# Performance work log

Hardware: AMD Instinct MI355X
Metric: run time of the kernel (lower is better)

Reference implementation:

```python
import jax, jax.numpy as jnp
import numpy as np
from jax import lax

NOISE_STD = 0.0005
ALPHA = 0.1
B, S, I, H, O = 128, 2000, 8, 512, 2
NUM_EXC, NUM_INH = 384, 128


def setup_inputs() -> dict:
    key = jax.random.key(0)
    ks = jax.random.split(key, 6)
    return {
        "input": jax.random.normal(ks[0], (B, S, I), dtype=jnp.float32),
        "noise": jax.random.normal(ks[1], (B, S, H), dtype=jnp.float32),
        "wi": jax.random.normal(ks[2], (I, H), dtype=jnp.float32) / np.sqrt(I),
        # excitatory rows in [0, 0.5], inhibitory rows in [-0.5, 0] (Dale's law)
        "wrec_exc": jax.random.uniform(ks[3], (NUM_EXC, H), dtype=jnp.float32, minval=0.0, maxval=0.5),
        "wrec_inh": jax.random.uniform(ks[4], (NUM_INH, H), dtype=jnp.float32, minval=-0.5, maxval=0.0),
        "wout": jax.random.normal(ks[5], (H, O), dtype=jnp.float32) / np.sqrt(H),
        "h0": jnp.zeros((H,), dtype=jnp.float32),
    }


def reference(input, noise, wi, wrec_exc, wrec_inh, wout, h0):
    batch = input.shape[0]
    # wrec rows: [exc sources; inh sources]
    wrec = jnp.concatenate([wrec_exc, wrec_inh], axis=0)  # [H, H]
    r0 = jnp.tanh(h0)  # [H]
    out0 = jnp.broadcast_to(r0 @ wout, (batch, wout.shape[1]))  # output[:, 0]
    h_init = jnp.broadcast_to(h0, (batch, h0.shape[0]))  # [B, H]
    # precompute input projection for steps 0..S-2 (last step's input unused)
    xproj = jnp.einsum("bsi,ih->sbh", input[:, :-1], wi)  # [S-1, B, H]
    noise_t = jnp.transpose(noise[:, :-1], (1, 0, 2))  # [S-1, B, H]

    def step(h, inp):
        x_t, n_t = inp
        r = jnp.tanh(h)
        h_new = h + NOISE_STD * n_t + ALPHA * (-h + r @ wrec.T + x_t)
        return h_new, jnp.tanh(h_new) @ wout  # emit output[:, i+1]

    _, outs = lax.scan(step, h_init, (xproj, noise_t))  # outs: [S-1, B, O]
    output = jnp.concatenate([out0[None], outs], axis=0)  # [S, B, O]
    return jnp.transpose(output, (1, 0, 2))  # [B, S, O]
```

## Files before the change

### kernel.cpp

```cpp
#include <hip/hip_runtime.h>
#include <cmath>


constexpr int kS = 2000, kI = 8, kH = 512, kO = 2;
constexpr float kNoiseStd = 0.0005f, kAlpha = 0.1f;

constexpr int GROUPS = 8;
constexpr int NSPL   = 2;
constexpr int JS     = 256;
constexpr int NTHR   = 512;
constexpr int NBLK   = GROUPS * NSPL;
constexpr int RSLOT  = 8192;

typedef _Float16 half8  __attribute__((ext_vector_type(8)));
typedef float    floatx4 __attribute__((ext_vector_type(4)));
typedef unsigned uintx4  __attribute__((ext_vector_type(4)));

#define MFMA16(A, B, C) __builtin_amdgcn_mfma_f32_16x16x32_f16((A), (B), (C), 0, 0, 0)
#define PIN8(a) asm volatile("" : "+v"((a)[0]), "+v"((a)[1]), "+v"((a)[2]), "+v"((a)[3]), \
                                   "+v"((a)[4]), "+v"((a)[5]), "+v"((a)[6]), "+v"((a)[7]))

static __device__ __forceinline__ unsigned ld_flag(const unsigned* p) {
  return __hip_atomic_load(p, __ATOMIC_RELAXED, __HIP_MEMORY_SCOPE_AGENT);
}
static __device__ __forceinline__ void st_flag(unsigned* p, unsigned v) {
  __hip_atomic_store(p, v, __ATOMIC_RELAXED, __HIP_MEMORY_SCOPE_AGENT);
}

static __device__ __forceinline__ float fast_tanh(float x) {
  const float ax = __builtin_fabsf(x);
  const float e = __builtin_amdgcn_exp2f(2.8853900817779268f * ax);
  const float r = __builtin_amdgcn_rcpf(e + 1.0f);
  return __builtin_copysignf(__builtin_fmaf(-2.0f, r, 1.0f), x);
}

__global__ __launch_bounds__(NTHR, 1) void rnn_k(
    const float* __restrict__ inp,
    const float* __restrict__ noise,
    const float* __restrict__ wi,
    const float* __restrict__ wexc,
    const float* __restrict__ winh,
    const float* __restrict__ wout,
    const float* __restrict__ h0,
    float* __restrict__ out,
    _Float16* __restrict__ rbuf,
    unsigned* __restrict__ flags)
{
  const int bid = blockIdx.x;
  const int g = bid & 7;
  const int c = bid >> 3;
  const int tid = threadIdx.x;
  const int w = tid >> 6;
  const int lane = tid & 63;
  const int l15 = lane & 15;
  const int lhi = lane >> 4;

  const int j0 = c * JS + w * 32 + l15;
  const int j1 = j0 + 16;
  const int ktp = c * 8 + w;
  const int jsub0 = l15 >> 3, jsub1 = 2 + (l15 >> 3), vv = l15 & 7;

  unsigned myXcd;
  asm volatile("s_getreg_b32 %0, hwreg(HW_REG_XCC_ID)" : "=s"(myXcd));
  myXcd &= 0x7fffu;

  __shared__ _Float16 ldsA[2][RSLOT];
  __shared__ half8 ws_wout[16][64];
  __shared__ float ldsIN[16][kI];

  half8 wfo0[8], wfo1[8], wfp0[8], wfp1[8];
  {
    const float* wr0 = (j0 < 384) ? (wexc + (size_t)j0 * kH) : (winh + (size_t)(j0 - 384) * kH);
    const float* wr1 = (j1 < 384) ? (wexc + (size_t)j1 * kH) : (winh + (size_t)(j1 - 384) * kH);
    const int ko = (c * 8) * 32 + lhi * 8;
    const int kp = ((c ^ 1) * 8) * 32 + lhi * 8;
#pragma unroll
    for (int t = 0; t < 8; ++t) {
      half8 a, b, d, e;
#pragma unroll
      for (int v = 0; v < 8; ++v) {
        a[v] = (_Float16)wr0[ko + t * 32 + v];
        b[v] = (_Float16)wr1[ko + t * 32 + v];
        d[v] = (_Float16)wr0[kp + t * 32 + v];
        e[v] = (_Float16)wr1[kp + t * 32 + v];
      }
      wfo0[t] = a; wfo1[t] = b; wfp0[t] = d; wfp1[t] = e;
    }
    PIN8(wfo0); PIN8(wfo1); PIN8(wfp0); PIN8(wfp1);
  }

  float wiv0[8], wiv1[8];
#pragma unroll
  for (int i = 0; i < 8; ++i) { wiv0[i] = wi[i * kH + j0]; wiv1[i] = wi[i * kH + j1]; }

  if (c == 0 && w < 4) {
#pragma unroll
    for (int t = 0; t < 4; ++t) {
      const int kt = w * 4 + t;
      const int k0 = kt * 32 + lhi * 8;
      half8 hv;
#pragma unroll
      for (int v = 0; v < 8; ++v)
        hv[v] = (l15 < kO) ? (_Float16)wout[(size_t)(k0 + v) * kO + l15] : (_Float16)0.f;
      ws_wout[kt][lane] = hv;
    }
  }

  float hq0[4], hq1[4];
  {
    const float h00 = h0[j0], h01 = h0[j1];
#pragma unroll
    for (int q = 0; q < 4; ++q) { hq0[q] = h00; hq1[q] = h01; }
    const _Float16 r00 = (_Float16)fast_tanh(h00);
    const _Float16 r01 = (_Float16)fast_tanh(h01);
#pragma unroll
    for (int q = 0; q < 4; ++q) {
      const int bb = lhi * 4 + q;
      ldsA[0][ktp * 512 + (bb + 16 * jsub0) * 8 + vv] = r00;
      ldsA[0][ktp * 512 + (bb + 16 * jsub1) * 8 + vv] = r01;
    }
    const uintx4 pub = *(const uintx4*)((const char*)&ldsA[0][0] + ktp * 1024 + lane * 16);
    char* dst = (char*)rbuf + (size_t)(0 * GROUPS + g) * (RSLOT * 2) + ktp * 1024 + lane * 16;
    asm volatile("global_store_dwordx4 %0, %1, off sc0 sc1" :: "v"(dst), "v"(pub) : "memory");
  }
  __syncthreads();
  if (tid == 0) st_flag(&flags[(0 * GROUPS + g) * NSPL + c], (myXcd << 16) | 1u);

  bool sameXcd;
  {
    unsigned pf;
    const unsigned* fp = &flags[(0 * GROUPS + g) * NSPL + (c ^ 1)];
    do { pf = ld_flag(fp); } while ((pf & 0xffffu) < 1u);
    sameXcd = ((pf >> 16) == myXcd);
    asm volatile("" ::: "memory");
  }

  for (int s = 0; s < kS; ++s) {
    const int cur = s & 1;
    const bool lastS = (s == kS - 1);
    if (lastS && c != 0) break;

    if (c == 0 && w == 7 && s > 0) {
      floatx4 oa = {0,0,0,0}, ob = {0,0,0,0};
      const char* bprev = (const char*)&ldsA[cur ^ 1][0];
#pragma unroll
      for (int kt = 0; kt < 16; kt += 2) {
        const half8 f0 = *(const half8*)(bprev + kt * 1024 + lane * 16);
        const half8 f1 = *(const half8*)(bprev + (kt + 1) * 1024 + lane * 16);
        oa = MFMA16(f0, ws_wout[kt][lane], oa);
        ob = MFMA16(f1, ws_wout[kt + 1][lane], ob);
      }
      if (l15 < kO) {
#pragma unroll
        for (int q = 0; q < 4; ++q)
          out[((size_t)(g * 16 + lhi * 4 + q) * kS + (s - 1)) * kO + l15] = oa[q] + ob[q];
      }
    }

    float nz0[4], nz1[4];
    float inv = 0.f;
    if (!lastS) {
#pragma unroll
      for (int q = 0; q < 4; ++q) {
        const int b = g * 16 + lhi * 4 + q;
        nz0[q] = noise[((size_t)b * kS + s) * kH + j0];
        nz1[q] = noise[((size_t)b * kS + s) * kH + j1];
      }
      if (w == 2 || w == 3) {
        const int ii = tid - 128;
        inv = inp[((size_t)(g * 16 + (ii >> 3)) * kS + s) * kI + (ii & 7)];
      }
    }

    {
      const unsigned need = (unsigned)(s + 1);
      const unsigned* fp = &flags[(cur * GROUPS + g) * NSPL + (c ^ 1)];
      while ((ld_flag(fp) & 0xffffu) < need) {}
      asm volatile("" ::: "memory");
    }

    uintx4 pv;
    {
      const char* src = (const char*)rbuf + (size_t)(cur * GROUPS + g) * (RSLOT * 2)
                        + (c ^ 1) * 8192 + tid * 16;
      if (sameXcd)
        asm volatile("global_load_dwordx4 %0, %1, off sc0" : "=&v"(pv) : "v"(src) : "memory");
      else
        asm volatile("global_load_dwordx4 %0, %1, off sc0 sc1" : "=&v"(pv) : "v"(src) : "memory");
    }

    floatx4 a00 = {0,0,0,0}, a01 = {0,0,0,0}, a10 = {0,0,0,0}, a11 = {0,0,0,0};
    const char* base = (const char*)&ldsA[cur][0];
    const char* baseO = base + c * 8192;
    const char* baseP = base + (c ^ 1) * 8192;
#pragma unroll
    for (int t = 0; t < 8; t += 2) {
      const half8 f0 = *(const half8*)(baseO + t * 1024 + lane * 16);
      const half8 f1 = *(const half8*)(baseO + (t + 1) * 1024 + lane * 16);
      a00 = MFMA16(f0, wfo0[t], a00);
      a10 = MFMA16(f0, wfo1[t], a10);
      a01 = MFMA16(f1, wfo0[t + 1], a01);
      a11 = MFMA16(f1, wfo1[t + 1], a11);
    }
    __builtin_amdgcn_sched_barrier(0);
    asm volatile("s_waitcnt vmcnt(0)" : "+v"(pv) :: "memory");
    *(uintx4*)((char*)&ldsA[cur][0] + (c ^ 1) * 8192 + tid * 16) = pv;
    if (!lastS && (w == 2 || w == 3)) {
      const int ii = tid - 128;
      ldsIN[ii >> 3][ii & 7] = inv;
    }
    __syncthreads();

#pragma unroll
    for (int t = 0; t < 8; t += 2) {
      const half8 f0 = *(const half8*)(baseP + t * 1024 + lane * 16);
      const half8 f1 = *(const half8*)(baseP + (t + 1) * 1024 + lane * 16);
      a00 = MFMA16(f0, wfp0[t], a00);
      a10 = MFMA16(f0, wfp1[t], a10);
      a01 = MFMA16(f1, wfp0[t + 1], a01);
      a11 = MFMA16(f1, wfp1[t + 1], a11);
    }

    if (!lastS) {
      _Float16* lA = &ldsA[cur ^ 1][0];
#pragma unroll
      for (int q = 0; q < 4; ++q) {
        const int bb = lhi * 4 + q;
        const floatx4 iv0 = *(const floatx4*)&ldsIN[bb][0];
        const floatx4 iv1 = *(const floatx4*)&ldsIN[bb][4];
        float x0 = 0.f, x1 = 0.f;
#pragma unroll
        for (int i = 0; i < 4; ++i) {
          x0 = fmaf(iv0[i], wiv0[i], x0); x0 = fmaf(iv1[i], wiv0[i + 4], x0);
          x1 = fmaf(iv0[i], wiv1[i], x1); x1 = fmaf(iv1[i], wiv1[i + 4], x1);
        }
        const float y0 = a00[q] + a01[q], y1 = a10[q] + a11[q];
        const float h0n = hq0[q] + kNoiseStd * nz0[q] + kAlpha * (-hq0[q] + y0 + x0);
        const float h1n = hq1[q] + kNoiseStd * nz1[q] + kAlpha * (-hq1[q] + y1 + x1);
        hq0[q] = h0n; hq1[q] = h1n;
        lA[ktp * 512 + (bb + 16 * jsub0) * 8 + vv] = (_Float16)fast_tanh(h0n);
        lA[ktp * 512 + (bb + 16 * jsub1) * 8 + vv] = (_Float16)fast_tanh(h1n);
      }
      const uintx4 pub = *(const uintx4*)((const char*)lA + ktp * 1024 + lane * 16);
      char* dst = (char*)rbuf + (size_t)((cur ^ 1) * GROUPS + g) * (RSLOT * 2)
                  + ktp * 1024 + lane * 16;
      if (sameXcd)
        asm volatile("global_store_dwordx4 %0, %1, off sc0" :: "v"(dst), "v"(pub) : "memory");
      else
        asm volatile("global_store_dwordx4 %0, %1, off sc0 sc1" :: "v"(dst), "v"(pub) : "memory");
    }
    __syncthreads();
    if (!lastS && tid == 0)
      st_flag(&flags[((cur ^ 1) * GROUPS + g) * NSPL + c], (unsigned)(s + 2));
  }

  if (c == 0 && w == 7) {
    const char* bfin = (const char*)&ldsA[(kS - 1) & 1][0];
    floatx4 oa = {0,0,0,0}, ob = {0,0,0,0};
#pragma unroll
    for (int kt = 0; kt < 16; kt += 2) {
      const half8 f0 = *(const half8*)(bfin + kt * 1024 + lane * 16);
      const half8 f1 = *(const half8*)(bfin + (kt + 1) * 1024 + lane * 16);
      oa = MFMA16(f0, ws_wout[kt][lane], oa);
      ob = MFMA16(f1, ws_wout[kt + 1][lane], ob);
    }
    if (l15 < kO) {
#pragma unroll
      for (int q = 0; q < 4; ++q)
        out[((size_t)(g * 16 + lhi * 4 + q) * kS + (kS - 1)) * kO + l15] = oa[q] + ob[q];
    }
  }
}

extern "C" void kernel_launch(void* const* d_in, const int* in_sizes, int n_in,
                              void* d_out, int out_size, void* d_ws, size_t ws_size,
                              hipStream_t stream) {
  const float* inp   = (const float*)d_in[0];
  const float* noise = (const float*)d_in[1];
  const float* wi    = (const float*)d_in[2];
  const float* wexc  = (const float*)d_in[3];
  const float* winh  = (const float*)d_in[4];
  const float* wout  = (const float*)d_in[5];
  const float* h0    = (const float*)d_in[6];

  _Float16* rbuf = (_Float16*)d_ws;
  const size_t rbytes = (size_t)2 * GROUPS * RSLOT * sizeof(_Float16);
  unsigned* flags = (unsigned*)((char*)d_ws + rbytes);

  hipMemsetAsync(flags, 0, 2 * GROUPS * NSPL * sizeof(unsigned), stream);
  rnn_k<<<NBLK, NTHR, 0, stream>>>(inp, noise, wi, wexc, winh, wout, h0,
                                   (float*)d_out, rbuf, flags);
}
```

Measured before the change: 4.531 ms.

## Remove mid-step barrier by loading peer fragments directly into registers

Each wave now loads the peer half of the recurrent activations straight from global memory into MFMA operand registers, instead of staging them in LDS and waiting on a mid-step __syncthreads. The LDS activation buffer becomes triple-buffered and the input slice is prefetched one step ahead into a double-buffered LDS array, so the per-step barrier is no longer needed. The goal is to shorten the serial critical path of each recurrence step. The cost is eight extra 16-byte global loads per lane per step and more live registers.

```diff
diff --git a/kernel.cpp b/kernel.cpp
--- a/kernel.cpp
+++ b/kernel.cpp
@@ -64,9 +64,9 @@
   asm volatile("s_getreg_b32 %0, hwreg(HW_REG_XCC_ID)" : "=s"(myXcd));
   myXcd &= 0x7fffu;
 
-  __shared__ _Float16 ldsA[2][RSLOT];
+  __shared__ _Float16 ldsA[3][RSLOT];
   __shared__ half8 ws_wout[16][64];
-  __shared__ float ldsIN[16][kI];
+  __shared__ float ldsIN[2][16][kI];
 
   half8 wfo0[8], wfo1[8], wfp0[8], wfp1[8];
   {
@@ -104,6 +104,11 @@
         hv[v] = (l15 < kO) ? (_Float16)wout[(size_t)(k0 + v) * kO + l15] : (_Float16)0.f;
       ws_wout[kt][lane] = hv;
     }
+  }
+
+  if (w == 2 || w == 3) {
+    const int ii = tid - 128;
+    ldsIN[0][ii >> 3][ii & 7] = inp[((size_t)(g * 16 + (ii >> 3)) * kS + 0) * kI + (ii & 7)];
   }
 
   float hq0[4], hq1[4];
@@ -135,6 +140,9 @@
     asm volatile("" ::: "memory");
   }
 
+  const char* base = (const char*)&ldsA[0][0];
+  int s3p = 2, s3c = 0, s3n = 1;
+
   for (int s = 0; s < kS; ++s) {
     const int cur = s & 1;
     const bool lastS = (s == kS - 1);
@@ -142,7 +150,7 @@
 
     if (c == 0 && w == 7 && s > 0) {
       floatx4 oa = {0,0,0,0}, ob = {0,0,0,0};
-      const char* bprev = (const char*)&ldsA[cur ^ 1][0];
+      const char* bprev = base + s3p * 16384;
 #pragma unroll
       for (int kt = 0; kt < 16; kt += 2) {
         const half8 f0 = *(const half8*)(bprev + kt * 1024 + lane * 16);
@@ -158,7 +166,7 @@
     }
 
     float nz0[4], nz1[4];
-    float inv = 0.f;
+    float invN = 0.f;
     if (!lastS) {
 #pragma unroll
       for (int q = 0; q < 4; ++q) {
@@ -166,10 +174,10 @@
         nz0[q] = noise[((size_t)b * kS + s) * kH + j0];
         nz1[q] = noise[((size_t)b * kS + s) * kH + j1];
       }
-      if (w == 2 || w == 3) {
-        const int ii = tid - 128;
-        inv = inp[((size_t)(g * 16 + (ii >> 3)) * kS + s) * kI + (ii & 7)];
-      }
+    }
+    if (s < kS - 2 && (w == 2 || w == 3)) {
+      const int ii = tid - 128;
+      invN = inp[((size_t)(g * 16 + (ii >> 3)) * kS + (s + 1)) * kI + (ii & 7)];
     }
 
     {
@@ -180,19 +188,51 @@
     }
 
     uintx4 pv;
+    half8 rf0, rf1, rf2, rf3, rf4, rf5, rf6, rf7;
     {
-      const char* src = (const char*)rbuf + (size_t)(cur * GROUPS + g) * (RSLOT * 2)
-                        + (c ^ 1) * 8192 + tid * 16;
-      if (sameXcd)
-        asm volatile("global_load_dwordx4 %0, %1, off sc0" : "=&v"(pv) : "v"(src) : "memory");
-      else
-        asm volatile("global_load_dwordx4 %0, %1, off sc0 sc1" : "=&v"(pv) : "v"(src) : "memory");
+      const char* phalf = (const char*)rbuf + (size_t)(cur * GROUPS + g) * (RSLOT * 2)
+                          + (c ^ 1) * 8192;
+      const char* srcpv = phalf + tid * 16;
+      const char* srcrf = phalf + lane * 16;
+      const char* srcrh = srcrf + 4096;
+      if (sameXcd) {
+        asm volatile("global_load_dwordx4 %0, %1, off sc0" : "=&v"(pv) : "v"(srcpv) : "memory");
+        asm volatile(
+          "global_load_dwordx4 %0, %4, off sc0\n\t"
+          "global_load_dwordx4 %1, %4, off offset:1024 sc0\n\t"
+          "global_load_dwordx4 %2, %4, off offset:2048 sc0\n\t"
+          "global_load_dwordx4 %3, %4, off offset:3072 sc0"
+          : "=&v"(rf0), "=&v"(rf1), "=&v"(rf2), "=&v"(rf3)
+          : "v"(srcrf) : "memory");
+        asm volatile(
+          "global_load_dwordx4 %0, %4, off sc0\n\t"
+          "global_load_dwordx4 %1, %4, off offset:1024 sc0\n\t"
+          "global_load_dwordx4 %2, %4, off offset:2048 sc0\n\t"
+          "global_load_dwordx4 %3, %4, off offset:3072 sc0"
+          : "=&v"(rf4), "=&v"(rf5), "=&v"(rf6), "=&v"(rf7)
+          : "v"(srcrh) : "memory");
+      } else {
+        asm volatile("global_load_dwordx4 %0, %1, off sc0 sc1" : "=&v"(pv) : "v"(srcpv) : "memory");
+        asm volatile(
+          "global_load_dwordx4 %0, %4, off sc0 sc1\n\t"
+          "global_load_dwordx4 %1, %4, off offset:1024 sc0 sc1\n\t"
+          "global_load_dwordx4 %2, %4, off offset:2048 sc0 sc1\n\t"
+          "global_load_dwordx4 %3, %4, off offset:3072 sc0 sc1"
+          : "=&v"(rf0), "=&v"(rf1), "=&v"(rf2), "=&v"(rf3)
+          : "v"(srcrf) : "memory");
+        asm volatile(
+          "global_load_dwordx4 %0, %4, off sc0 sc1\n\t"
+          "global_load_dwordx4 %1, %4, off offset:1024 sc0 sc1\n\t"
+          "global_load_dwordx4 %2, %4, off offset:2048 sc0 sc1\n\t"
+          "global_load_dwordx4 %3, %4, off offset:3072 sc0 sc1"
+          : "=&v"(rf4), "=&v"(rf5), "=&v"(rf6), "=&v"(rf7)
+          : "v"(srcrh) : "memory");
+      }
     }
 
     floatx4 a00 = {0,0,0,0}, a01 = {0,0,0,0}, a10 = {0,0,0,0}, a11 = {0,0,0,0};
-    const char* base = (const char*)&ldsA[cur][0];
-    const char* baseO = base + c * 8192;
-    const char* baseP = base + (c ^ 1) * 8192;
+    const char* bA = base + s3c * 16384;
+    const char* baseO = bA + c * 8192;
 #pragma unroll
     for (int t = 0; t < 8; t += 2) {
       const half8 f0 = *(const half8*)(baseO + t * 1024 + lane * 16);
@@ -203,31 +243,40 @@
       a11 = MFMA16(f1, wfo1[t + 1], a11);
     }
     __builtin_amdgcn_sched_barrier(0);
-    asm volatile("s_waitcnt vmcnt(0)" : "+v"(pv) :: "memory");
-    *(uintx4*)((char*)&ldsA[cur][0] + (c ^ 1) * 8192 + tid * 16) = pv;
-    if (!lastS && (w == 2 || w == 3)) {
+    asm volatile("s_waitcnt vmcnt(0)"
+                 : "+v"(pv), "+v"(rf0), "+v"(rf1), "+v"(rf2), "+v"(rf3),
+                   "+v"(rf4), "+v"(rf5), "+v"(rf6), "+v"(rf7) :: "memory");
+    __builtin_amdgcn_sched_barrier(0);
+    *(uintx4*)((char*)base + s3c * 16384 + (c ^ 1) * 8192 + tid * 16) = pv;
+    if (s < kS - 2 && (w == 2 || w == 3)) {
       const int ii = tid - 128;
-      ldsIN[ii >> 3][ii & 7] = inv;
-    }
-    __syncthreads();
-
-#pragma unroll
-    for (int t = 0; t < 8; t += 2) {
-      const half8 f0 = *(const half8*)(baseP + t * 1024 + lane * 16);
-      const half8 f1 = *(const half8*)(baseP + (t + 1) * 1024 + lane * 16);
-      a00 = MFMA16(f0, wfp0[t], a00);
-      a10 = MFMA16(f0, wfp1[t], a10);
-      a01 = MFMA16(f1, wfp0[t + 1], a01);
-      a11 = MFMA16(f1, wfp1[t + 1], a11);
-    }
+      ldsIN[(s + 1) & 1][ii >> 3][ii & 7] = invN;
+    }
+
+    a00 = MFMA16(rf0, wfp0[0], a00);
+    a10 = MFMA16(rf0, wfp1[0], a10);
+    a01 = MFMA16(rf1, wfp0[1], a01);
+    a11 = MFMA16(rf1, wfp1[1], a11);
+    a00 = MFMA16(rf2, wfp0[2], a00);
+    a10 = MFMA16(rf2, wfp1[2], a10);
+    a01 = MFMA16(rf3, wfp0[3], a01);
+    a11 = MFMA16(rf3, wfp1[3], a11);
+    a00 = MFMA16(rf4, wfp0[4], a00);
+    a10 = MFMA16(rf4, wfp1[4], a10);
+    a01 = MFMA16(rf5, wfp0[5], a01);
+    a11 = MFMA16(rf5, wfp1[5], a11);
+    a00 = MFMA16(rf6, wfp0[6], a00);
+    a10 = MFMA16(rf6, wfp1[6], a10);
+    a01 = MFMA16(rf7, wfp0[7], a01);
+    a11 = MFMA16(rf7, wfp1[7], a11);
 
     if (!lastS) {
-      _Float16* lA = &ldsA[cur ^ 1][0];
+      _Float16* lA = &ldsA[0][0] + s3n * RSLOT;
 #pragma unroll
       for (int q = 0; q < 4; ++q) {
         const int bb = lhi * 4 + q;
-        const floatx4 iv0 = *(const floatx4*)&ldsIN[bb][0];
-        const floatx4 iv1 = *(const floatx4*)&ldsIN[bb][4];
+        const floatx4 iv0 = *(const floatx4*)&ldsIN[s & 1][bb][0];
+        const floatx4 iv1 = *(const floatx4*)&ldsIN[s & 1][bb][4];
         float x0 = 0.f, x1 = 0.f;
 #pragma unroll
         for (int i = 0; i < 4; ++i) {
@@ -252,10 +301,12 @@
     __syncthreads();
     if (!lastS && tid == 0)
       st_flag(&flags[((cur ^ 1) * GROUPS + g) * NSPL + c], (unsigned)(s + 2));
+
+    const int t3 = s3p; s3p = s3c; s3c = s3n; s3n = t3;
   }
 
   if (c == 0 && w == 7) {
-    const char* bfin = (const char*)&ldsA[(kS - 1) & 1][0];
+    const char* bfin = base + ((kS - 1) % 3) * 16384;
     floatx4 oa = {0,0,0,0}, ob = {0,0,0,0};
 #pragma unroll
     for (int kt = 0; kt < 16; kt += 2) {
```

Measured after the change: 5.161 ms. +13.9%, slower.

## Have each block interleave two batch groups to overlap cross-block waits

Applied to the files above, without the earlier changes.

Only 8 of the 16 launched blocks stay active. Each one now handles two batch groups (p and p+4) and alternates between them within every timestep, keeping separate LDS buffers, hidden state and flags per group. The aim is to hide the peer-flag wait and global exchange latency of one group behind the MFMA work of the other. The cost is half as many active CUs, double the serial work per block and more LDS. The first-step sameXcd detection only checks group p's flag.

```diff
diff --git a/kernel.cpp b/kernel.cpp
--- a/kernel.cpp
+++ b/kernel.cpp
@@ -9,7 +9,7 @@
 constexpr int NSPL   = 2;
 constexpr int JS     = 256;
 constexpr int NTHR   = 512;
-constexpr int NBLK   = GROUPS * NSPL;
+constexpr int NBLK   = 16;
 constexpr int RSLOT  = 8192;
 
 typedef _Float16 half8  __attribute__((ext_vector_type(8)));
@@ -47,7 +47,8 @@
     unsigned* __restrict__ flags)
 {
   const int bid = blockIdx.x;
-  const int g = bid & 7;
+  if ((bid & 7) >= 4) return;
+  const int p = bid & 3;
   const int c = bid >> 3;
   const int tid = threadIdx.x;
   const int w = tid >> 6;
@@ -64,9 +65,9 @@
   asm volatile("s_getreg_b32 %0, hwreg(HW_REG_XCC_ID)" : "=s"(myXcd));
   myXcd &= 0x7fffu;
 
-  __shared__ _Float16 ldsA[2][RSLOT];
+  __shared__ _Float16 ldsA[2][2][RSLOT];
   __shared__ half8 ws_wout[16][64];
-  __shared__ float ldsIN[16][kI];
+  __shared__ float ldsIN[2][16][kI];
 
   half8 wfo0[8], wfo1[8], wfp0[8], wfp1[8];
   {
@@ -106,30 +107,37 @@
     }
   }
 
-  float hq0[4], hq1[4];
+  float hq0[2][4], hq1[2][4];
   {
     const float h00 = h0[j0], h01 = h0[j1];
-#pragma unroll
-    for (int q = 0; q < 4; ++q) { hq0[q] = h00; hq1[q] = h01; }
     const _Float16 r00 = (_Float16)fast_tanh(h00);
     const _Float16 r01 = (_Float16)fast_tanh(h01);
 #pragma unroll
-    for (int q = 0; q < 4; ++q) {
-      const int bb = lhi * 4 + q;
-      ldsA[0][ktp * 512 + (bb + 16 * jsub0) * 8 + vv] = r00;
-      ldsA[0][ktp * 512 + (bb + 16 * jsub1) * 8 + vv] = r01;
-    }
-    const uintx4 pub = *(const uintx4*)((const char*)&ldsA[0][0] + ktp * 1024 + lane * 16);
-    char* dst = (char*)rbuf + (size_t)(0 * GROUPS + g) * (RSLOT * 2) + ktp * 1024 + lane * 16;
-    asm volatile("global_store_dwordx4 %0, %1, off sc0 sc1" :: "v"(dst), "v"(pub) : "memory");
+    for (int gi = 0; gi < 2; ++gi) {
+      const int gg = p + gi * 4;
+#pragma unroll
+      for (int q = 0; q < 4; ++q) { hq0[gi][q] = h00; hq1[gi][q] = h01; }
+#pragma unroll
+      for (int q = 0; q < 4; ++q) {
+        const int bb = lhi * 4 + q;
+        ldsA[gi][0][ktp * 512 + (bb + 16 * jsub0) * 8 + vv] = r00;
+        ldsA[gi][0][ktp * 512 + (bb + 16 * jsub1) * 8 + vv] = r01;
+      }
+      const uintx4 pub = *(const uintx4*)((const char*)&ldsA[gi][0][0] + ktp * 1024 + lane * 16);
+      char* dst = (char*)rbuf + (size_t)(0 * GROUPS + gg) * (RSLOT * 2) + ktp * 1024 + lane * 16;
+      asm volatile("global_store_dwordx4 %0, %1, off sc0 sc1" :: "v"(dst), "v"(pub) : "memory");
+    }
   }
   __syncthreads();
-  if (tid == 0) st_flag(&flags[(0 * GROUPS + g) * NSPL + c], (myXcd << 16) | 1u);
+  if (tid == 0) {
+    st_flag(&flags[(0 * GROUPS + p) * NSPL + c], (myXcd << 16) | 1u);
+    st_flag(&flags[(0 * GROUPS + (p + 4)) * NSPL + c], (myXcd << 16) | 1u);
+  }
 
   bool sameXcd;
   {
     unsigned pf;
-    const unsigned* fp = &flags[(0 * GROUPS + g) * NSPL + (c ^ 1)];
+    const unsigned* fp = &flags[(0 * GROUPS + p) * NSPL + (c ^ 1)];
     do { pf = ld_flag(fp); } while ((pf & 0xffffu) < 1u);
     sameXcd = ((pf >> 16) == myXcd);
     asm volatile("" ::: "memory");
@@ -140,134 +148,143 @@
     const bool lastS = (s == kS - 1);
     if (lastS && c != 0) break;
 
-    if (c == 0 && w == 7 && s > 0) {
+#pragma unroll
+    for (int gi = 0; gi < 2; ++gi) {
+      const int gg = p + gi * 4;
+
+      if (c == 0 && w == 7 && s > 0) {
+        floatx4 oa = {0,0,0,0}, ob = {0,0,0,0};
+        const char* bprev = (const char*)&ldsA[gi][cur ^ 1][0];
+#pragma unroll
+        for (int kt = 0; kt < 16; kt += 2) {
+          const half8 f0 = *(const half8*)(bprev + kt * 1024 + lane * 16);
+          const half8 f1 = *(const half8*)(bprev + (kt + 1) * 1024 + lane * 16);
+          oa = MFMA16(f0, ws_wout[kt][lane], oa);
+          ob = MFMA16(f1, ws_wout[kt + 1][lane], ob);
+        }
+        if (l15 < kO) {
+#pragma unroll
+          for (int q = 0; q < 4; ++q)
+            out[((size_t)(gg * 16 + lhi * 4 + q) * kS + (s - 1)) * kO + l15] = oa[q] + ob[q];
+        }
+      }
+
+      float nz0[4], nz1[4];
+      float inv = 0.f;
+      if (!lastS) {
+#pragma unroll
+        for (int q = 0; q < 4; ++q) {
+          const int b = gg * 16 + lhi * 4 + q;
+          nz0[q] = noise[((size_t)b * kS + s) * kH + j0];
+          nz1[q] = noise[((size_t)b * kS + s) * kH + j1];
+        }
+        if (w == 2 || w == 3) {
+          const int ii = tid - 128;
+          inv = inp[((size_t)(gg * 16 + (ii >> 3)) * kS + s) * kI + (ii & 7)];
+        }
+      }
+
+      {
+        const unsigned need = (unsigned)(s + 1);
+        const unsigned* fp = &flags[(cur * GROUPS + gg) * NSPL + (c ^ 1)];
+        while ((ld_flag(fp) & 0xffffu) < need) {}
+        asm volatile("" ::: "memory");
+      }
+
+      uintx4 pv;
+      {
+        const char* src = (const char*)rbuf + (size_t)(cur * GROUPS + gg) * (RSLOT * 2)
+                          + (c ^ 1) * 8192 + tid * 16;
+        if (sameXcd)
+          asm volatile("global_load_dwordx4 %0, %1, off sc0" : "=&v"(pv) : "v"(src) : "memory");
+        else
+          asm volatile("global_load_dwordx4 %0, %1, off sc0 sc1" : "=&v"(pv) : "v"(src) : "memory");
+      }
+
+      floatx4 a00 = {0,0,0,0}, a01 = {0,0,0,0}, a10 = {0,0,0,0}, a11 = {0,0,0,0};
+      const char* base = (const char*)&ldsA[gi][cur][0];
+      const char* baseO = base + c * 8192;
+      const char* baseP = base + (c ^ 1) * 8192;
+#pragma unroll
+      for (int t = 0; t < 8; t += 2) {
+        const half8 f0 = *(const half8*)(baseO + t * 1024 + lane * 16);
+        const half8 f1 = *(const half8*)(baseO + (t + 1) * 1024 + lane * 16);
+        a00 = MFMA16(f0, wfo0[t], a00);
+        a10 = MFMA16(f0, wfo1[t], a10);
+        a01 = MFMA16(f1, wfo0[t + 1], a01);
+        a11 = MFMA16(f1, wfo1[t + 1], a11);
+      }
+      __builtin_amdgcn_sched_barrier(0);
+      asm volatile("s_waitcnt vmcnt(0)" : "+v"(pv) :: "memory");
+      *(uintx4*)((char*)&ldsA[gi][cur][0] + (c ^ 1) * 8192 + tid * 16) = pv;
+      if (!lastS && (w == 2 || w == 3)) {
+        const int ii = tid - 128;
+        ldsIN[gi][ii >> 3][ii & 7] = inv;
+      }
+      __syncthreads();
+
+#pragma unroll
+      for (int t = 0; t < 8; t += 2) {
+        const half8 f0 = *(const half8*)(baseP + t * 1024 + lane * 16);
+        const half8 f1 = *(const half8*)(baseP + (t + 1) * 1024 + lane * 16);
+        a00 = MFMA16(f0, wfp0[t], a00);
+        a10 = MFMA16(f0, wfp1[t], a10);
+        a01 = MFMA16(f1, wfp0[t + 1], a01);
+        a11 = MFMA16(f1, wfp1[t + 1], a11);
+      }
+
+      if (!lastS) {
+        _Float16* lA = &ldsA[gi][cur ^ 1][0];
+#pragma unroll
+        for (int q = 0; q < 4; ++q) {
+          const int bb = lhi * 4 + q;
+          const floatx4 iv0 = *(const floatx4*)&ldsIN[gi][bb][0];
+          const floatx4 iv1 = *(const floatx4*)&ldsIN[gi][bb][4];
+          float x0 = 0.f, x1 = 0.f;
+#pragma unroll
+          for (int i = 0; i < 4; ++i) {
+            x0 = fmaf(iv0[i], wiv0[i], x0); x0 = fmaf(iv1[i], wiv0[i + 4], x0);
+            x1 = fmaf(iv0[i], wiv1[i], x1); x1 = fmaf(iv1[i], wiv1[i + 4], x1);
+          }
+          const float y0 = a00[q] + a01[q], y1 = a10[q] + a11[q];
+          const float h0n = hq0[gi][q] + kNoiseStd * nz0[q] + kAlpha * (-hq0[gi][q] + y0 + x0);
+          const float h1n = hq1[gi][q] + kNoiseStd * nz1[q] + kAlpha * (-hq1[gi][q] + y1 + x1);
+          hq0[gi][q] = h0n; hq1[gi][q] = h1n;
+          lA[ktp * 512 + (bb + 16 * jsub0) * 8 + vv] = (_Float16)fast_tanh(h0n);
+          lA[ktp * 512 + (bb + 16 * jsub1) * 8 + vv] = (_Float16)fast_tanh(h1n);
+        }
+        const uintx4 pub = *(const uintx4*)((const char*)lA + ktp * 1024 + lane * 16);
+        char* dst = (char*)rbuf + (size_t)((cur ^ 1) * GROUPS + gg) * (RSLOT * 2)
+                    + ktp * 1024 + lane * 16;
+        if (sameXcd)
+          asm volatile("global_store_dwordx4 %0, %1, off sc0" :: "v"(dst), "v"(pub) : "memory");
+        else
+          asm volatile("global_store_dwordx4 %0, %1, off sc0 sc1" :: "v"(dst), "v"(pub) : "memory");
+      }
+      __syncthreads();
+      if (!lastS && tid == 0)
+        st_flag(&flags[((cur ^ 1) * GROUPS + gg) * NSPL + c], (unsigned)(s + 2));
+    }
+  }
+
+  if (c == 0 && w == 7) {
+#pragma unroll
+    for (int gi = 0; gi < 2; ++gi) {
+      const int gg = p + gi * 4;
+      const char* bfin = (const char*)&ldsA[gi][(kS - 1) & 1][0];
       floatx4 oa = {0,0,0,0}, ob = {0,0,0,0};
-      const char* bprev = (const char*)&ldsA[cur ^ 1][0];
 #pragma unroll
       for (int kt = 0; kt < 16; kt += 2) {
-        const half8 f0 = *(const half8*)(bprev + kt * 1024 + lane * 16);
-        const half8 f1 = *(const half8*)(bprev + (kt + 1) * 1024 + lane * 16);
+        const half8 f0 = *(const half8*)(bfin + kt * 1024 + lane * 16);
+        const half8 f1 = *(const half8*)(bfin + (kt + 1) * 1024 + lane * 16);
         oa = MFMA16(f0, ws_wout[kt][lane], oa);
         ob = MFMA16(f1, ws_wout[kt + 1][lane], ob);
       }
       if (l15 < kO) {
 #pragma unroll
         for (int q = 0; q < 4; ++q)
-          out[((size_t)(g * 16 + lhi * 4 + q) * kS + (s - 1)) * kO + l15] = oa[q] + ob[q];
-      }
-    }
-
-    float nz0[4], nz1[4];
-    float inv = 0.f;
-    if (!lastS) {
-#pragma unroll
-      for (int q = 0; q < 4; ++q) {
-        const int b = g * 16 + lhi * 4 + q;
-        nz0[q] = noise[((size_t)b * kS + s) * kH + j0];
-        nz1[q] = noise[((size_t)b * kS + s) * kH + j1];
-      }
-      if (w == 2 || w == 3) {
-        const int ii = tid - 128;
-        inv = inp[((size_t)(g * 16 + (ii >> 3)) * kS + s) * kI + (ii & 7)];
-      }
-    }
-
-    {
-      const unsigned need = (unsigned)(s + 1);
-      const unsigned* fp = &flags[(cur * GROUPS + g) * NSPL + (c ^ 1)];
-      while ((ld_flag(fp) & 0xffffu) < need) {}
-      asm volatile("" ::: "memory");
-    }
-
-    uintx4 pv;
-    {
-      const char* src = (const char*)rbuf + (size_t)(cur * GROUPS + g) * (RSLOT * 2)
-                        + (c ^ 1) * 8192 + tid * 16;
-      if (sameXcd)
-        asm volatile("global_load_dwordx4 %0, %1, off sc0" : "=&v"(pv) : "v"(src) : "memory");
-      else
-        asm volatile("global_load_dwordx4 %0, %1, off sc0 sc1" : "=&v"(pv) : "v"(src) : "memory");
-    }
-
-    floatx4 a00 = {0,0,0,0}, a01 = {0,0,0,0}, a10 = {0,0,0,0}, a11 = {0,0,0,0};
-    const char* base = (const char*)&ldsA[cur][0];
-    const char* baseO = base + c * 8192;
-    const char* baseP = base + (c ^ 1) * 8192;
-#pragma unroll
-    for (int t = 0; t < 8; t += 2) {
-      const half8 f0 = *(const half8*)(baseO + t * 1024 + lane * 16);
-      const half8 f1 = *(const half8*)(baseO + (t + 1) * 1024 + lane * 16);
-      a00 = MFMA16(f0, wfo0[t], a00);
-      a10 = MFMA16(f0, wfo1[t], a10);
-      a01 = MFMA16(f1, wfo0[t + 1], a01);
-      a11 = MFMA16(f1, wfo1[t + 1], a11);
-    }
-    __builtin_amdgcn_sched_barrier(0);
-    asm volatile("s_waitcnt vmcnt(0)" : "+v"(pv) :: "memory");
-    *(uintx4*)((char*)&ldsA[cur][0] + (c ^ 1) * 8192 + tid * 16) = pv;
-    if (!lastS && (w == 2 || w == 3)) {
-      const int ii = tid - 128;
-      ldsIN[ii >> 3][ii & 7] = inv;
-    }
-    __syncthreads();
-
-#pragma unroll
-    for (int t = 0; t < 8; t += 2) {
-      const half8 f0 = *(const half8*)(baseP + t * 1024 + lane * 16);
-      const half8 f1 = *(const half8*)(baseP + (t + 1) * 1024 + lane * 16);
-      a00 = MFMA16(f0, wfp0[t], a00);
-      a10 = MFMA16(f0, wfp1[t], a10);
-      a01 = MFMA16(f1, wfp0[t + 1], a01);
-      a11 = MFMA16(f1, wfp1[t + 1], a11);
-    }
-
-    if (!lastS) {
-      _Float16* lA = &ldsA[cur ^ 1][0];
-#pragma unroll
-      for (int q = 0; q < 4; ++q) {
-        const int bb = lhi * 4 + q;
-        const floatx4 iv0 = *(const floatx4*)&ldsIN[bb][0];
-        const floatx4 iv1 = *(const floatx4*)&ldsIN[bb][4];
-        float x0 = 0.f, x1 = 0.f;
-#pragma unroll
-        for (int i = 0; i < 4; ++i) {
-          x0 = fmaf(iv0[i], wiv0[i], x0); x0 = fmaf(iv1[i], wiv0[i + 4], x0);
-          x1 = fmaf(iv0[i], wiv1[i], x1); x1 = fmaf(iv1[i], wiv1[i + 4], x1);
-        }
-        const float y0 = a00[q] + a01[q], y1 = a10[q] + a11[q];
-        const float h0n = hq0[q] + kNoiseStd * nz0[q] + kAlpha * (-hq0[q] + y0 + x0);
-        const float h1n = hq1[q] + kNoiseStd * nz1[q] + kAlpha * (-hq1[q] + y1 + x1);
-        hq0[q] = h0n; hq1[q] = h1n;
-        lA[ktp * 512 + (bb + 16 * jsub0) * 8 + vv] = (_Float16)fast_tanh(h0n);
-        lA[ktp * 512 + (bb + 16 * jsub1) * 8 + vv] = (_Float16)fast_tanh(h1n);
-      }
-      const uintx4 pub = *(const uintx4*)((const char*)lA + ktp * 1024 + lane * 16);
-      char* dst = (char*)rbuf + (size_t)((cur ^ 1) * GROUPS + g) * (RSLOT * 2)
-                  + ktp * 1024 + lane * 16;
-      if (sameXcd)
-        asm volatile("global_store_dwordx4 %0, %1, off sc0" :: "v"(dst), "v"(pub) : "memory");
-      else
-        asm volatile("global_store_dwordx4 %0, %1, off sc0 sc1" :: "v"(dst), "v"(pub) : "memory");
-    }
-    __syncthreads();
-    if (!lastS && tid == 0)
-      st_flag(&flags[((cur ^ 1) * GROUPS + g) * NSPL + c], (unsigned)(s + 2));
-  }
-
-  if (c == 0 && w == 7) {
-    const char* bfin = (const char*)&ldsA[(kS - 1) & 1][0];
-    floatx4 oa = {0,0,0,0}, ob = {0,0,0,0};
-#pragma unroll
-    for (int kt = 0; kt < 16; kt += 2) {
-      const half8 f0 = *(const half8*)(bfin + kt * 1024 + lane * 16);
-      const half8 f1 = *(const half8*)(bfin + (kt + 1) * 1024 + lane * 16);
-      oa = MFMA16(f0, ws_wout[kt][lane], oa);
-      ob = MFMA16(f1, ws_wout[kt + 1][lane], ob);
-    }
-    if (l15 < kO) {
-#pragma unroll
-      for (int q = 0; q < 4; ++q)
-        out[((size_t)(g * 16 + lhi * 4 + q) * kS + (kS - 1)) * kO + l15] = oa[q] + ob[q];
+          out[((size_t)(gg * 16 + lhi * 4 + q) * kS + (kS - 1)) * kO + l15] = oa[q] + ob[q];
+      }
     }
   }
 }
```

New measurement: 10.36 ms. 129% more time.
